# Kernel optimization log

Hardware: AMD Instinct MI355X
Metric: run time of the kernel (lower is better)

The kernel has to match this reference:

```python
import jax, jax.numpy as jnp
import numpy as np

B, N, K = 2, 2048, 30          # batch, residues, neighbors
DN, DE, L = 256, 128, 3        # dim_nodes, dim_edges, num_layers
NF, EF = 12, 28                # raw node / edge feature dims
EPS = 1e-6


def _gather(h, idx):
    # h: [B,N,D], idx: [B,N,K] -> [B,N,K,D]
    b, n, k = idx.shape
    d = h.shape[-1]
    return jnp.take_along_axis(h, idx.reshape(b, n * k, 1), axis=1).reshape(b, n, k, d)


def _nrm(v):
    return v / (jnp.linalg.norm(v, axis=-1, keepdims=True) + EPS)


def _forward(X, C, Wn, bn, We, be, Wm1, bm1, Wm2, bm2, Wue1, bue1, Wue2, bue2):
    mask_i = (C > 0).astype(X.dtype)                      # [B,N]
    Nat, CA, Cat, Oat = X[..., 0, :], X[..., 1, :], X[..., 2, :], X[..., 3, :]

    # local residue frames via Gram-Schmidt on (N, CA, C)
    u = _nrm(Cat - CA)
    v0 = Nat - CA
    v = _nrm(v0 - jnp.sum(v0 * u, -1, keepdims=True) * u)
    w = jnp.cross(u, v)
    R = jnp.stack([u, v, w], axis=-1)                     # [B,N,3,3]

    # node features: internal coords (unit bond vectors + log lengths)
    def bond_feat(bv):
        return jnp.concatenate([_nrm(bv), jnp.log(jnp.linalg.norm(bv, axis=-1, keepdims=True) + EPS)], -1)
    node_feat = jnp.concatenate([bond_feat(CA - Nat), bond_feat(Cat - CA), bond_feat(Oat - Cat)], -1)  # [B,N,12]
    node_h = (node_feat @ Wn + bn) * mask_i[..., None]

    # kNN graph on centroid distances (graph_distance_atom_type=-1)
    Xc = X.mean(axis=2)                                   # [B,N,3]
    D2 = jnp.sum((Xc[:, :, None] - Xc[:, None, :]) ** 2, -1)  # [B,N,N]
    BIG = 1e9
    D2 = D2 + BIG * (1.0 - mask_i)[:, None, :] + BIG * jnp.eye(N, dtype=X.dtype)[None]
    _, edge_idx = jax.lax.top_k(-D2, K)                   # [B,N,K]

    mask_j = _gather(mask_i[..., None], edge_idx)[..., 0]
    mask_ij = mask_i[..., None] * mask_j                  # [B,N,K]

    # edge features: RBF distances + local-frame direction + relative rotation
    xj = _gather(Xc, edge_idx)
    d = xj - Xc[:, :, None]                               # [B,N,K,3]
    dist = jnp.linalg.norm(d, axis=-1)
    local = jnp.einsum('bndc,bnkd->bnkc', R, d)           # R_i^T d
    dirv = local / (dist[..., None] + EPS)
    Rj = _gather(R.reshape(B, N, 9), edge_idx).reshape(B, N, K, 3, 3)
    Rrel = jnp.einsum('bnde,bnkdf->bnkef', R, Rj).reshape(B, N, K, 9)  # R_i^T R_j
    centers = jnp.linspace(0.0, 20.0, 16)
    sigma = 20.0 / 16.0
    rbf = jnp.exp(-(((dist[..., None] - centers) / sigma) ** 2))       # [B,N,K,16]
    edge_h = (jnp.concatenate([rbf, dirv, Rrel], -1) @ We + be) * mask_ij[..., None]

    # GNN message passing: gather -> MLP -> masked mean scatter, + edge update
    denom = jnp.sum(mask_ij, -1, keepdims=True) + EPS     # [B,N,1]
    for l in range(L):
        hj = _gather(node_h, edge_idx)                    # [B,N,K,DN]
        hi = jnp.broadcast_to(node_h[:, :, None], hj.shape)
        mi = jnp.concatenate([hi, hj, edge_h], -1)        # [B,N,K,2*DN+DE]
        m = jax.nn.softplus(mi @ Wm1[l] + bm1[l]) @ Wm2[l] + bm2[l]
        m = m * mask_ij[..., None]
        node_h = (node_h + m.sum(axis=2) / denom) * mask_i[..., None]
        e = jax.nn.softplus(mi @ Wue1[l] + bue1[l]) @ Wue2[l] + bue2[l]
        edge_h = (edge_h + e) * mask_ij[..., None]

    return node_h, edge_h, edge_idx, mask_i, mask_ij


def setup_inputs() -> dict:
    key = jax.random.key(0)
    ks = jax.random.split(key, 10)
    s = lambda i, shp: jax.random.normal(ks[i], shp, jnp.float32) * 0.05
    M = 2 * DN + DE
    inp = {
        'X': jax.random.normal(ks[0], (B, N, 4, 3), jnp.float32),
        'C': jax.random.randint(ks[1], (B, N), 0, 4),
        'Wn': s(2, (NF, DN)), 'bn': jnp.zeros((DN,), jnp.float32),
        'We': s(3, (EF, DE)), 'be': jnp.zeros((DE,), jnp.float32),
        'Wm1': s(4, (L, M, DN)), 'bm1': jnp.zeros((L, DN), jnp.float32),
        'Wm2': s(5, (L, DN, DN)), 'bm2': jnp.zeros((L, DN), jnp.float32),
        'Wue1': s(6, (L, M, DE)), 'bue1': jnp.zeros((L, DE), jnp.float32),
        'Wue2': s(7, (L, DE, DE)), 'bue2': jnp.zeros((L, DE), jnp.float32),
    }
    return inp


def reference(X, C, Wn, bn, We, be, Wm1, bm1, Wm2, bm2, Wue1, bue1, Wue2, bue2):
    return _forward(X, C, Wn, bn, We, be, Wm1, bm1, Wm2, bm2, Wue1, bue1, Wue2, bue2)
```

## Files before the change

### kernel.cpp

```cpp
#include <hip/hip_runtime.h>
#include <math.h>

#define Bdim 2
#define Nn   2048
#define Kn   30
#define KP   32
#define DNc  256
#define DEc  128
#define NODES (Bdim*Nn)
#define EDGES (Bdim*Nn*Kn)
#define RPAD  (NODES*KP)
#define EPSF 1e-6f

#define BK 64
#define LDA (BK+8)
#define LDA0 40
#define LDP 136

typedef __attribute__((ext_vector_type(8))) short short8;
typedef __attribute__((ext_vector_type(4))) short sh4;
typedef __attribute__((ext_vector_type(4))) float floatx4;

__device__ __forceinline__ float softplusf(float x){
    float e = __expf(-fabsf(x));
    return fmaxf(x, 0.f) + __logf(1.f + e);
}

__device__ __forceinline__ unsigned short f2bf(float x){
    union { float f; unsigned u; } v; v.f = x;
    unsigned r = v.u + 0x7fff + ((v.u >> 16) & 1);
    return (unsigned short)(r >> 16);
}
__device__ __forceinline__ float bf2f(unsigned short h){
    union { unsigned u; float f; } v; v.u = ((unsigned)h) << 16;
    return v.f;
}

__global__ __launch_bounds__(256) void k_geom(
    const float* __restrict__ X, const int* __restrict__ C,
    float* __restrict__ Xc, float* __restrict__ Rm,
    float* __restrict__ feat, float* __restrict__ mask_out)
{
    int id = blockIdx.x*256 + threadIdx.x;
    if (id >= NODES) return;
    float a[4][3];
    #pragma unroll
    for (int t=0;t<4;++t)
        #pragma unroll
        for (int d=0;d<3;++d) a[t][d] = X[id*12 + t*3 + d];
    #pragma unroll
    for (int d=0; d<3; ++d){
        float s = __fadd_rn(__fadd_rn(__fadd_rn(a[0][d],a[1][d]),a[2][d]),a[3][d]);
        Xc[id*3+d] = __fmul_rn(s, 0.25f);
    }
    mask_out[id] = (C[id] > 0) ? 1.f : 0.f;

    float u[3], v[3], w[3], b2[3], v0[3], vv[3];
    #pragma unroll
    for (int d=0;d<3;++d) b2[d] = a[2][d]-a[1][d];
    float n2 = sqrtf(b2[0]*b2[0]+b2[1]*b2[1]+b2[2]*b2[2]);
    #pragma unroll
    for (int d=0;d<3;++d) u[d] = b2[d]/(n2+EPSF);
    #pragma unroll
    for (int d=0;d<3;++d) v0[d] = a[0][d]-a[1][d];
    float dt = v0[0]*u[0]+v0[1]*u[1]+v0[2]*u[2];
    #pragma unroll
    for (int d=0;d<3;++d) vv[d] = v0[d] - dt*u[d];
    float nv = sqrtf(vv[0]*vv[0]+vv[1]*vv[1]+vv[2]*vv[2]);
    #pragma unroll
    for (int d=0;d<3;++d) v[d] = vv[d]/(nv+EPSF);
    w[0] = u[1]*v[2]-u[2]*v[1];
    w[1] = u[2]*v[0]-u[0]*v[2];
    w[2] = u[0]*v[1]-u[1]*v[0];
    #pragma unroll
    for (int d=0;d<3;++d){
        Rm[id*9 + d*3 + 0] = u[d];
        Rm[id*9 + d*3 + 1] = v[d];
        Rm[id*9 + d*3 + 2] = w[d];
    }
    float bonds[3][3];
    #pragma unroll
    for (int d=0;d<3;++d){
        bonds[0][d] = a[1][d]-a[0][d];
        bonds[1][d] = b2[d];
        bonds[2][d] = a[3][d]-a[2][d];
    }
    #pragma unroll
    for (int bi=0;bi<3;++bi){
        float nb = sqrtf(bonds[bi][0]*bonds[bi][0]+bonds[bi][1]*bonds[bi][1]+bonds[bi][2]*bonds[bi][2]);
        #pragma unroll
        for (int d=0;d<3;++d) feat[id*12 + bi*4 + d] = bonds[bi][d]/(nb+EPSF);
        feat[id*12 + bi*4 + 3] = logf(nb+EPSF);
    }
}

__global__ __launch_bounds__(256) void k_nodeh(
    const float* __restrict__ feat, const float* __restrict__ Wn,
    const float* __restrict__ bn, const int* __restrict__ C,
    float* __restrict__ node_h, unsigned short* __restrict__ node_bf)
{
    int nid = blockIdx.x;
    int c   = threadIdx.x;
    __shared__ float f[12];
    if (c < 12) f[c] = feat[nid*12 + c];
    __syncthreads();
    float acc = bn[c];
    #pragma unroll
    for (int k=0;k<12;++k) acc += f[k]*Wn[k*DNc + c];
    float mask = (C[nid] > 0) ? 1.f : 0.f;
    float r = acc*mask;
    node_h[nid*DNc + c] = r;
    node_bf[nid*DNc + c] = f2bf(r);
}

__global__ __launch_bounds__(256) void k_knn(
    const float* __restrict__ Xc, const int* __restrict__ C,
    int* __restrict__ eidx, float* __restrict__ eidx_f)
{
    __shared__ float sx[Nn], sy[Nn], sz[Nn], sadd[Nn];
    int tid  = threadIdx.x;
    int lane = tid & 63, wave = tid >> 6;
    int node0 = blockIdx.x*4;
    int base  = (node0 >> 11) << 11;
    for (int j=tid; j<Nn; j+=256){
        int gj = base + j;
        sx[j] = Xc[gj*3+0]; sy[j] = Xc[gj*3+1]; sz[j] = Xc[gj*3+2];
        sadd[j] = (C[gj] > 0) ? 0.f : 1e9f;
    }
    __syncthreads();

    int node = node0 + wave;
    int iloc = node & (Nn-1);
    float xi = sx[iloc], yi = sy[iloc], zi = sz[iloc];

    unsigned long long kreg[32];
    unsigned long long gm[8];
    #pragma unroll
    for (int t=0; t<32; ++t){
        int j = lane + t*64;
        float dx = __fsub_rn(xi, sx[j]);
        float dy = __fsub_rn(yi, sy[j]);
        float dz = __fsub_rn(zi, sz[j]);
        float vv = __fadd_rn(__fadd_rn(__fmul_rn(dx,dx),__fmul_rn(dy,dy)),__fmul_rn(dz,dz));
        vv = __fadd_rn(vv, sadd[j]);
        if (j == iloc) vv = __fadd_rn(vv, 1e9f);
        union { float f; unsigned u; } cv; cv.f = vv;
        kreg[t] = (((unsigned long long)cv.u) << 11) | (unsigned)j;
    }
    #pragma unroll
    for (int g=0; g<8; ++g){
        unsigned long long a = kreg[4*g+0], b = kreg[4*g+1];
        unsigned long long c = kreg[4*g+2], d = kreg[4*g+3];
        unsigned long long m1 = a<b?a:b, m2 = c<d?c:d;
        gm[g] = m1<m2?m1:m2;
    }
    unsigned long long m = gm[0]; int marg = 0;
    #pragma unroll
    for (int g=1; g<8; ++g) if (gm[g] < m){ m = gm[g]; marg = g; }

    for (int kk=0; kk<Kn; ++kk){
        unsigned long long best = m;
        #pragma unroll
        for (int d=1; d<64; d<<=1){
            unsigned long long o = __shfl_xor(best, d, 64);
            if (o < best) best = o;
        }
        if (lane == 0){
            int j = (int)(best & 2047ull);
            eidx  [(size_t)node*Kn + kk] = j;
            eidx_f[(size_t)node*Kn + kk] = (float)j;
        }
        if (m == best){
            #pragma unroll
            for (int g=0; g<8; ++g){
                if (marg == g){
                    #pragma unroll
                    for (int t=0; t<4; ++t)
                        if (kreg[4*g+t] == best) kreg[4*g+t] = ~0ull;
                    unsigned long long a = kreg[4*g+0], b = kreg[4*g+1];
                    unsigned long long c = kreg[4*g+2], d = kreg[4*g+3];
                    unsigned long long m1 = a<b?a:b, m2 = c<d?c:d;
                    gm[g] = m1<m2?m1:m2;
                }
            }
            m = gm[0]; marg = 0;
            #pragma unroll
            for (int g=1; g<8; ++g) if (gm[g] < m){ m = gm[g]; marg = g; }
        }
    }
}

__global__ __launch_bounds__(256) void k_edge_feat(
    const float* __restrict__ Xc, const float* __restrict__ Rm,
    const int* __restrict__ eidx, const int* __restrict__ C,
    unsigned short* __restrict__ featp,
    float* __restrict__ mask_ij_out, float* __restrict__ mask_pad,
    int* __restrict__ jg_pad, float* __restrict__ cnt)
{
    int r   = blockIdx.x*256 + threadIdx.x;
    int nid = r >> 5;
    int k   = r & 31;
    int b   = nid >> 11;
    float mij = 0.f;
    int   jb  = nid;
    float f[28];
    if (k < Kn){
        int e = nid*Kn + k;
        int j = eidx[e];
        jb = (b<<11) + j;
        mij = (C[nid] > 0 && C[jb] > 0) ? 1.f : 0.f;
        mask_ij_out[e] = mij;
        float xi0 = Xc[nid*3+0], xi1 = Xc[nid*3+1], xi2 = Xc[nid*3+2];
        float d0  = Xc[jb*3+0]-xi0;
        float d1  = Xc[jb*3+1]-xi1;
        float d2v = Xc[jb*3+2]-xi2;
        float dist = sqrtf(d0*d0 + d1*d1 + d2v*d2v);
        float ri[9], rj[9];
        #pragma unroll
        for (int q=0;q<9;++q) ri[q] = Rm[nid*9+q];
        #pragma unroll
        for (int q=0;q<9;++q) rj[q] = Rm[jb*9+q];
        #pragma unroll
        for (int c=0; c<16; ++c){
            float ctr = (20.f/15.f)*(float)c;
            float t = (dist - ctr)*(1.f/1.25f);
            f[c] = expf(-t*t);
        }
        #pragma unroll
        for (int cc=0; cc<3; ++cc){
            float loc = ri[0*3+cc]*d0 + ri[1*3+cc]*d1 + ri[2*3+cc]*d2v;
            f[16+cc] = loc/(dist+EPSF);
        }
        #pragma unroll
        for (int ee=0; ee<3; ++ee)
            #pragma unroll
            for (int ff=0; ff<3; ++ff)
                f[19+ee*3+ff] = ri[0+ee]*rj[0+ff] + ri[3+ee]*rj[3+ff] + ri[6+ee]*rj[6+ff];
    }
    jg_pad[r]   = jb;
    mask_pad[r] = mij;

    unsigned long long bal = __ballot(mij > 0.f);
    int lane = threadIdx.x & 63;
    if (lane == 0)  cnt[r >> 5] = (float)__popcll(bal & 0xFFFFFFFFull);
    if (lane == 32) cnt[r >> 5] = (float)__popcll(bal >> 32);

    unsigned short ov[32];
    #pragma unroll
    for (int q=0;q<32;++q) ov[q] = 0;
    if (k < Kn){
        #pragma unroll
        for (int q=0;q<28;++q) ov[q] = f2bf(f[q]);
    }
    unsigned short* dst = featp + (size_t)r*32;
    #pragma unroll
    for (int q=0; q<4; ++q){
        short8 sv;
        #pragma unroll
        for (int z=0; z<8; ++z) sv[z] = (short)ov[q*8+z];
        *(short8*)(dst + q*8) = sv;
    }
}

__global__ __launch_bounds__(256) void k_edge0(
    const unsigned short* __restrict__ featp, const unsigned short* __restrict__ Wp,
    const float* __restrict__ be, const float* __restrict__ mask_pad,
    unsigned short* __restrict__ edge_pad)
{
    __shared__ __align__(16) unsigned short smem[128*LDP];
    __shared__ float smask[128];
    unsigned short* Als  = smem;
    unsigned short* Bls  = smem + 128*LDA0;
    unsigned short* tile = smem;

    int tid = threadIdx.x;
    int lane = tid & 63, wave = tid >> 6;
    int wm = wave >> 1, wn = wave & 1;

    {
        const unsigned short* Ab = featp + (size_t)blockIdx.x*128*32;
        #pragma unroll
        for (int it=0; it<2; ++it){
            int idx = it*256 + tid;
            int row = idx >> 2, q = idx & 3;
            *(float4*)(&Als[row*LDA0 + q*8]) = *(const float4*)(Ab + row*32 + q*8);
        }
        if (tid < 128){
            int row = tid;
            *(float4*)(&Bls[row*LDA0 + 0])  = *(const float4*)(Wp + row*32 + 0);
            *(float4*)(&Bls[row*LDA0 + 8])  = *(const float4*)(Wp + row*32 + 8);
            *(float4*)(&Bls[row*LDA0 + 16]) = *(const float4*)(Wp + row*32 + 16);
            *(float4*)(&Bls[row*LDA0 + 24]) = *(const float4*)(Wp + row*32 + 24);
        } else {
            smask[tid-128] = mask_pad[blockIdx.x*128 + (tid-128)];
        }
    }
    __syncthreads();

    floatx4 acc[4][4];
    #pragma unroll
    for (int i=0;i<4;++i)
        #pragma unroll
        for (int j=0;j<4;++j) acc[i][j] = (floatx4){0.f,0.f,0.f,0.f};
    short8 af[4], bf[4];
    int kidx = (lane>>4)*8;
    #pragma unroll
    for (int t=0;t<4;++t){
        int row = wm*64 + t*16 + (lane&15);
        af[t] = *(const short8*)(&Als[row*LDA0 + kidx]);
        int col = wn*64 + t*16 + (lane&15);
        bf[t] = *(const short8*)(&Bls[col*LDA0 + kidx]);
    }
    __syncthreads();
    #pragma unroll
    for (int i=0;i<4;++i)
        #pragma unroll
        for (int j=0;j<4;++j)
            acc[i][j] = __builtin_amdgcn_mfma_f32_16x16x32_bf16(bf[j], af[i], acc[i][j], 0,0,0);

    int quad = lane >> 4, cl = lane & 15;
    #pragma unroll
    for (int i=0;i<4;++i){
        int rowl = wm*64 + i*16 + cl;
        float mk = smask[rowl];
        #pragma unroll
        for (int j=0;j<4;++j){
            int coll = wn*64 + j*16 + quad*4;
            float4 bv = *(const float4*)&be[coll];
            sh4 w;
            w[0] = (short)f2bf((acc[i][j][0] + bv.x)*mk);
            w[1] = (short)f2bf((acc[i][j][1] + bv.y)*mk);
            w[2] = (short)f2bf((acc[i][j][2] + bv.z)*mk);
            w[3] = (short)f2bf((acc[i][j][3] + bv.w)*mk);
            *(sh4*)(&tile[rowl*LDP + coll]) = w;
        }
    }
    __syncthreads();
    {
        int rl = tid >> 1;
        int h  = tid & 1;
        unsigned short* dst = edge_pad + (size_t)(blockIdx.x*128 + rl)*128 + h*64;
        #pragma unroll
        for (int q=0; q<8; ++q)
            *(short8*)(dst + q*8) = *(const short8*)(&tile[rl*LDP + h*64 + q*8]);
    }
}

__global__ __launch_bounds__(256) void k_pack_all(
    const float* __restrict__ We, const float* __restrict__ Wm1,
    const float* __restrict__ Wue1, const float* __restrict__ Wue2,
    const float* __restrict__ Wm2,
    unsigned short* __restrict__ wWe0, unsigned short* __restrict__ wPQw,
    unsigned short* __restrict__ wEw, unsigned short* __restrict__ wUe2w,
    unsigned short* __restrict__ wM2w)
{
    int id = blockIdx.x*256 + threadIdx.x;
    if (id < 4096){
        int n = id >> 5, kk = id & 31;
        wWe0[id] = (kk < 28) ? f2bf(We[kk*128 + n]) : 0;
        return;
    }
    id -= 4096;
    if (id < 3*768*256){
        int l = id / (768*256);
        int rem = id % (768*256);
        int n = rem >> 8, k = rem & 255;
        int c = (n < 384) ? n : n - 384;
        int r = (n < 384) ? k : 256 + k;
        float v = (c < 256) ? Wm1[((size_t)l*640 + r)*256 + c]
                            : Wue1[((size_t)l*640 + r)*128 + (c-256)];
        wPQw[id] = f2bf(v);
        return;
    }
    id -= 3*768*256;
    if (id < 3*384*128){
        int l = id / (384*128);
        int rem = id % (384*128);
        int n = rem >> 7, k = rem & 127;
        int r = 512 + k;
        float v = (n < 256) ? Wm1[((size_t)l*640 + r)*256 + n]
                            : Wue1[((size_t)l*640 + r)*128 + (n-256)];
        wEw[id] = f2bf(v);
        return;
    }
    id -= 3*384*128;
    if (id < 3*128*128){
        int l = id / (128*128);
        int rem = id % (128*128);
        int n = rem >> 7, k = rem & 127;
        wUe2w[id] = f2bf(Wue2[((size_t)l*128 + k)*128 + n]);
        return;
    }
    id -= 3*128*128;
    if (id < 3*256*256){
        int l = id / (256*256);
        int rem = id % (256*256);
        int n = rem >> 8, k = rem & 255;
        wM2w[id] = f2bf(Wm2[((size_t)l*256 + k)*256 + n]);
    }
}

template<int NR>
__device__ __forceinline__ void stage_tile_t(
    const unsigned short* __restrict__ gbase, int ldg, int k0,
    unsigned short* lds, int tid)
{
    #pragma unroll
    for (int it=0; it<NR/32; ++it){
        int idx = it*256 + tid;
        int row = idx >> 3;
        int ke  = (idx & 7) * 8;
        const float4* src = (const float4*)(gbase + (size_t)row*ldg + k0 + ke);
        *(float4*)(&lds[row*LDA + ke]) = *src;
    }
}

template<int TI, int TJ>
__device__ __forceinline__ void mma_tile_t(
    const unsigned short* Als, const unsigned short* Bls,
    int wm, int wn, int lane, floatx4 acc[TI][TJ])
{
    #pragma unroll
    for (int s=0; s<2; ++s){
        short8 af[TI], bf[TJ];
        int kidx = s*32 + (lane>>4)*8;
        #pragma unroll
        for (int t=0;t<TI;++t){
            int row = wm*(TI*16) + t*16 + (lane&15);
            af[t] = *(const short8*)(&Als[row*LDA + kidx]);
        }
        #pragma unroll
        for (int t=0;t<TJ;++t){
            int col = wn*(TJ*16) + t*16 + (lane&15);
            bf[t] = *(const short8*)(&Bls[col*LDA + kidx]);
        }
        #pragma unroll
        for (int i=0;i<TI;++i)
            #pragma unroll
            for (int j=0;j<TJ;++j)
                acc[i][j] = __builtin_amdgcn_mfma_f32_16x16x32_bf16(af[i], bf[j], acc[i][j], 0,0,0);
    }
}

template<int TI, int TJ>
__device__ __forceinline__ void mma_tile_sw(
    const unsigned short* Als, const unsigned short* Bls,
    int wm, int wn, int lane, floatx4 acc[TI][TJ])
{
    #pragma unroll
    for (int s=0; s<2; ++s){
        short8 af[TI], bf[TJ];
        int kidx = s*32 + (lane>>4)*8;
        #pragma unroll
        for (int t=0;t<TI;++t){
            int row = wm*(TI*16) + t*16 + (lane&15);
            af[t] = *(const short8*)(&Als[row*LDA + kidx]);
        }
        #pragma unroll
        for (int t=0;t<TJ;++t){
            int col = wn*(TJ*16) + t*16 + (lane&15);
            bf[t] = *(const short8*)(&Bls[col*LDA + kidx]);
        }
        #pragma unroll
        for (int i=0;i<TI;++i)
            #pragma unroll
            for (int j=0;j<TJ;++j)
                acc[i][j] = __builtin_amdgcn_mfma_f32_16x16x32_bf16(bf[j], af[i], acc[i][j], 0,0,0);
    }
}

__device__ __forceinline__ void mma_tileA_gB(
    const unsigned short* Atile, const unsigned short* __restrict__ Bg,
    int k0, int wm, int wn, int lane, floatx4 acc[4][4])
{
    #pragma unroll
    for (int s=0; s<2; ++s){
        short8 af[4], bf[4];
        int kloc = s*32 + (lane>>4)*8;
        #pragma unroll
        for (int t=0;t<4;++t){
            int row = wm*64 + t*16 + (lane&15);
            af[t] = *(const short8*)(&Atile[row*LDP + k0 + kloc]);
            int col = wn*64 + t*16 + (lane&15);
            bf[t] = *(const short8*)(Bg + (size_t)col*128 + k0 + kloc);
        }
        #pragma unroll
        for (int i=0;i<4;++i)
            #pragma unroll
            for (int j=0;j<4;++j)
                acc[i][j] = __builtin_amdgcn_mfma_f32_16x16x32_bf16(af[i], bf[j], acc[i][j], 0,0,0);
    }
}

__global__ __launch_bounds__(256) void k_pq(
    const unsigned short* __restrict__ A, const unsigned short* __restrict__ Bw,
    unsigned short* __restrict__ PQbf,
    const float* __restrict__ bm1l, const float* __restrict__ bue1l)
{
    __shared__ __align__(16) unsigned short smem[2*64*LDA];
    unsigned short* Als = smem;
    unsigned short* Bls = smem + 64*LDA;
    unsigned short* tile = smem;
    int tid = threadIdx.x;
    int lane = tid & 63, wave = tid >> 6;
    int wm = wave >> 1, wn = wave & 1;
    const unsigned short* Ab = A + (size_t)blockIdx.x*64*256;
    const unsigned short* Bb = Bw + (size_t)blockIdx.y*64*256;
    floatx4 acc[2][2];
    #pragma unroll
    for (int i=0;i<2;++i)
        #pragma unroll
        for (int j=0;j<2;++j) acc[i][j] = (floatx4){0.f,0.f,0.f,0.f};
    for (int k0=0; k0<256; k0+=BK){
        stage_tile_t<64>(Ab, 256, k0, Als, tid);
        stage_tile_t<64>(Bb, 256, k0, Bls, tid);
        __syncthreads();
        mma_tile_sw<2,2>(Als, Bls, wm, wn, lane, acc);
        __syncthreads();
    }
    int quad = lane >> 4, cl = lane & 15;
    #pragma unroll
    for (int i=0;i<2;++i){
        int rowl = wm*32 + i*16 + cl;
        #pragma unroll
        for (int j=0;j<2;++j){
            int coll = wn*32 + j*16 + quad*4;
            int col0 = blockIdx.y*64 + coll;
            float4 bv;
            if (col0 < 256)      bv = *(const float4*)&bm1l[col0];
            else if (col0 < 384) bv = *(const float4*)&bue1l[col0-256];
            else                 bv = (float4){0.f,0.f,0.f,0.f};
            sh4 w;
            w[0] = (short)f2bf(acc[i][j][0] + bv.x);
            w[1] = (short)f2bf(acc[i][j][1] + bv.y);
            w[2] = (short)f2bf(acc[i][j][2] + bv.z);
            w[3] = (short)f2bf(acc[i][j][3] + bv.w);
            *(sh4*)(&tile[rowl*LDP + coll]) = w;
        }
    }
    __syncthreads();
    {
        int rl = tid >> 2;
        int h  = tid & 3;
        unsigned short* dst = PQbf + (size_t)(blockIdx.x*64 + rl)*768 + blockIdx.y*64 + h*16;
        *(short8*)(dst + 0) = *(const short8*)(&tile[rl*LDP + h*16 + 0]);
        *(short8*)(dst + 8) = *(const short8*)(&tile[rl*LDP + h*16 + 8]);
    }
}

__global__ __launch_bounds__(256) void k_h1s(
    const unsigned short* __restrict__ Apad, const unsigned short* __restrict__ Bw,
    const unsigned short* __restrict__ PQbf, const int* __restrict__ jg_pad,
    const float* __restrict__ mask_pad,
    unsigned short* __restrict__ Sout)
{
    __shared__ __align__(16) unsigned short smem[2*128*LDA];
    __shared__ float smask[128];
    unsigned short* Als = smem;
    unsigned short* Bls = smem + 128*LDA;
    unsigned short* pqT = smem;

    int tid = threadIdx.x;
    int lane = tid & 63, wave = tid >> 6;
    int wm = wave >> 1, wn = wave & 1;
    int colblk = blockIdx.y;

    const unsigned short* Ab = Apad + (size_t)blockIdx.x*128*128;
    const unsigned short* Bb = Bw + (size_t)colblk*128*128;
    floatx4 acc[4][4];
    #pragma unroll
    for (int i=0;i<4;++i)
        #pragma unroll
        for (int j=0;j<4;++j) acc[i][j] = (floatx4){0.f,0.f,0.f,0.f};
    for (int k0=0; k0<128; k0+=BK){
        stage_tile_t<128>(Ab, 128, k0, Als, tid);
        stage_tile_t<128>(Bb, 128, k0, Bls, tid);
        __syncthreads();
        mma_tile_t<4,4>(Als, Bls, wm, wn, lane, acc);
        __syncthreads();
    }

    {
        int colbase = colblk*128;
        #pragma unroll
        for (int it=0; it<2; ++it){
            int w    = it*256 + tid;
            int rq   = w & 31;
            int c8   = w >> 5;
            int row0 = rq*4;
            int r0   = blockIdx.x*128 + row0;
            int ni   = r0 >> 5;
            int4 jg4 = *(const int4*)&jg_pad[r0];
            int colg = colbase + c8*8;
            short8 pv = *(const short8*)(PQbf + (size_t)ni*768 + colg);
            short8 q0 = *(const short8*)(PQbf + (size_t)jg4.x*768 + 384 + colg);
            short8 q1 = *(const short8*)(PQbf + (size_t)jg4.y*768 + 384 + colg);
            short8 q2 = *(const short8*)(PQbf + (size_t)jg4.z*768 + 384 + colg);
            short8 q3 = *(const short8*)(PQbf + (size_t)jg4.w*768 + 384 + colg);
            #pragma unroll
            for (int q=0; q<8; ++q){
                float pf = bf2f((unsigned short)pv[q]);
                sh4 ov;
                ov[0] = (short)f2bf(pf + bf2f((unsigned short)q0[q]));
                ov[1] = (short)f2bf(pf + bf2f((unsigned short)q1[q]));
                ov[2] = (short)f2bf(pf + bf2f((unsigned short)q2[q]));
                ov[3] = (short)f2bf(pf + bf2f((unsigned short)q3[q]));
                *(sh4*)(&pqT[(c8*8 + q)*LDP + row0]) = ov;
            }
        }
        if (tid < 128) smask[tid] = mask_pad[blockIdx.x*128 + tid];
    }
    __syncthreads();

    int quad = lane >> 4, cl = lane & 15;
    float sumA[4] = {0.f,0.f,0.f,0.f};
    float sumB[4] = {0.f,0.f,0.f,0.f};
    #pragma unroll
    for (int i=0;i<4;++i){
        int rowl0 = wm*64 + i*16 + quad*4;
        float4 mk = *(const float4*)&smask[rowl0];
        float mkv[4] = {mk.x, mk.y, mk.z, mk.w};
        #pragma unroll
        for (int j=0;j<4;++j){
            int coll = wn*64 + j*16 + cl;
            sh4 pq4 = *(const sh4*)(&pqT[coll*LDP + rowl0]);
            #pragma unroll
            for (int rg=0; rg<4; ++rg){
                float v  = softplusf(acc[i][j][rg] + bf2f((unsigned short)pq4[rg]));
                float mv = mkv[rg]*v;
                if (i < 2) sumA[j] += mv; else sumB[j] += mv;
            }
        }
    }

    int nodeA = blockIdx.x*4 + wm*2;
    #pragma unroll
    for (int j=0;j<4;++j){
        float a = sumA[j];
        a += __shfl_xor(a, 16, 64);
        a += __shfl_xor(a, 32, 64);
        float b = sumB[j];
        b += __shfl_xor(b, 16, 64);
        b += __shfl_xor(b, 32, 64);
        int col = colblk*128 + wn*64 + j*16 + cl;
        if (quad == 0)      Sout[(size_t)nodeA*256 + col]     = f2bf(a);
        else if (quad == 1) Sout[(size_t)(nodeA+1)*256 + col] = f2bf(b);
    }
}

__global__ __launch_bounds__(256) void k_h1e(
    const unsigned short* __restrict__ Apad, const unsigned short* __restrict__ BwE,
    const unsigned short* __restrict__ BwU2,
    const unsigned short* __restrict__ PQbf, const int* __restrict__ jg_pad,
    const float* __restrict__ mask_pad, const float* __restrict__ bue2l,
    unsigned short* __restrict__ edge_pad, float* __restrict__ edge_f32,
    int last)
{
    __shared__ __align__(16) unsigned short smem[2*128*LDA];
    __shared__ float sbias[128];
    unsigned short* Als  = smem;
    unsigned short* Bls  = smem + 128*LDA;
    unsigned short* tile = smem;

    int tid = threadIdx.x;
    int lane = tid & 63, wave = tid >> 6;
    int wm = wave >> 1, wn = wave & 1;

    if (tid < 128) sbias[tid] = bue2l[tid];

    const unsigned short* Ab = Apad + (size_t)blockIdx.x*128*128;
    floatx4 acc[4][4];
    #pragma unroll
    for (int i=0;i<4;++i)
        #pragma unroll
        for (int j=0;j<4;++j) acc[i][j] = (floatx4){0.f,0.f,0.f,0.f};
    for (int k0=0; k0<128; k0+=BK){
        stage_tile_t<128>(Ab, 128, k0, Als, tid);
        stage_tile_t<128>(BwE, 128, k0, Bls, tid);
        __syncthreads();
        mma_tile_t<4,4>(Als, Bls, wm, wn, lane, acc);
        __syncthreads();
    }

    {
        int rl = tid >> 1;
        int h  = tid & 1;
        int r  = blockIdx.x*128 + rl;
        int ni = r >> 5;
        int jg = jg_pad[r];
        int cb = 256 + h*64;
        const unsigned short* Pr = PQbf + (size_t)ni*768 + cb;
        const unsigned short* Qr = PQbf + (size_t)jg*768 + 384 + cb;
        #pragma unroll
        for (int q=0; q<8; ++q){
            short8 pv = *(const short8*)(Pr + q*8);
            short8 qv = *(const short8*)(Qr + q*8);
            short8 ov;
            #pragma unroll
            for (int z=0; z<8; ++z)
                ov[z] = (short)f2bf(bf2f((unsigned short)pv[z]) + bf2f((unsigned short)qv[z]));
            *(short8*)(&tile[rl*LDP + h*64 + q*8]) = ov;
        }
    }
    __syncthreads();

    int quad = lane >> 4, cl = lane & 15;
    #pragma unroll
    for (int i=0;i<4;++i){
        #pragma unroll
        for (int rg=0;rg<4;++rg){
            int rowl = wm*64 + i*16 + quad*4 + rg;
            #pragma unroll
            for (int j=0;j<4;++j){
                int coll = wn*64 + j*16 + cl;
                float pq = bf2f(tile[rowl*LDP + coll]);
                float v  = softplusf(acc[i][j][rg] + pq);
                tile[rowl*LDP + coll] = f2bf(v);
            }
        }
    }
    __syncthreads();

    floatx4 acc2[4][4];
    #pragma unroll
    for (int i=0;i<4;++i)
        #pragma unroll
        for (int j=0;j<4;++j) acc2[i][j] = (floatx4){0.f,0.f,0.f,0.f};
    mma_tileA_gB(tile, BwU2, 0,  wm, wn, lane, acc2);
    mma_tileA_gB(tile, BwU2, 64, wm, wn, lane, acc2);
    __syncthreads();

    #pragma unroll
    for (int i=0;i<4;++i){
        #pragma unroll
        for (int rg=0;rg<4;++rg){
            int rowl = wm*64 + i*16 + quad*4 + rg;
            #pragma unroll
            for (int j=0;j<4;++j){
                int coll = wn*64 + j*16 + cl;
                tile[rowl*LDP + coll] = f2bf(acc2[i][j][rg]);
            }
        }
    }
    __syncthreads();

    if (last){
        int c16  = lane & 31;
        int rsub = lane >> 5;
        #pragma unroll
        for (int step=0; step<16; ++step){
            int rowl = wave*32 + step*2 + rsub;
            int R = blockIdx.x*128 + rowl;
            int k = R & (KP-1);
            if (k < Kn){
                float mij = mask_pad[R];
                int node = R >> 5;
                int e = node*Kn + k;
                sh4 ov = *(const sh4*)(edge_pad + (size_t)R*128 + c16*4);
                sh4 av = *(const sh4*)(&tile[rowl*LDP + c16*4]);
                float4 bv = *(const float4*)(&sbias[c16*4]);
                float4 f;
                f.x = (bf2f((unsigned short)ov[0]) + bf2f((unsigned short)av[0]) + bv.x)*mij;
                f.y = (bf2f((unsigned short)ov[1]) + bf2f((unsigned short)av[1]) + bv.y)*mij;
                f.z = (bf2f((unsigned short)ov[2]) + bf2f((unsigned short)av[2]) + bv.z)*mij;
                f.w = (bf2f((unsigned short)ov[3]) + bf2f((unsigned short)av[3]) + bv.w)*mij;
                *(float4*)(edge_f32 + (size_t)e*128 + c16*4) = f;
            }
        }
    } else {
        int c8   = lane & 15;
        int rsub = lane >> 4;
        #pragma unroll
        for (int step=0; step<8; ++step){
            int rowl = wave*32 + step*4 + rsub;
            int R = blockIdx.x*128 + rowl;
            int k = R & (KP-1);
            if (k < Kn){
                float mij = mask_pad[R];
                unsigned short* ep = edge_pad + (size_t)R*128 + c8*8;
                short8 ov = *(const short8*)ep;
                short8 av = *(const short8*)(&tile[rowl*LDP + c8*8]);
                float4 b0 = *(const float4*)(&sbias[c8*8]);
                float4 b1 = *(const float4*)(&sbias[c8*8 + 4]);
                float nv[8];
                nv[0] = (bf2f((unsigned short)ov[0]) + bf2f((unsigned short)av[0]) + b0.x)*mij;
                nv[1] = (bf2f((unsigned short)ov[1]) + bf2f((unsigned short)av[1]) + b0.y)*mij;
                nv[2] = (bf2f((unsigned short)ov[2]) + bf2f((unsigned short)av[2]) + b0.z)*mij;
                nv[3] = (bf2f((unsigned short)ov[3]) + bf2f((unsigned short)av[3]) + b0.w)*mij;
                nv[4] = (bf2f((unsigned short)ov[4]) + bf2f((unsigned short)av[4]) + b1.x)*mij;
                nv[5] = (bf2f((unsigned short)ov[5]) + bf2f((unsigned short)av[5]) + b1.y)*mij;
                nv[6] = (bf2f((unsigned short)ov[6]) + bf2f((unsigned short)av[6]) + b1.z)*mij;
                nv[7] = (bf2f((unsigned short)ov[7]) + bf2f((unsigned short)av[7]) + b1.w)*mij;
                short8 sv;
                #pragma unroll
                for (int z=0; z<8; ++z) sv[z] = (short)f2bf(nv[z]);
                *(short8*)ep = sv;
            }
        }
    }
}

__global__ __launch_bounds__(256) void k_node_gemm(
    const unsigned short* __restrict__ S, const unsigned short* __restrict__ Bw,
    const float* __restrict__ bm2l, const float* __restrict__ cnt,
    const float* __restrict__ mask_i,
    float* __restrict__ node_h, unsigned short* __restrict__ node_bf)
{
    __shared__ __align__(16) unsigned short Als[32*LDA];
    __shared__ __align__(16) unsigned short Bls[64*LDA];
    int tid = threadIdx.x;
    int lane = tid & 63, wave = tid >> 6;
    int wm = wave >> 1, wn = wave & 1;
    const unsigned short* Ab = S + (size_t)blockIdx.x*32*256;
    const unsigned short* Bb = Bw + (size_t)blockIdx.y*64*256;
    floatx4 acc[1][2];
    acc[0][0] = (floatx4){0.f,0.f,0.f,0.f};
    acc[0][1] = (floatx4){0.f,0.f,0.f,0.f};
    for (int k0=0; k0<256; k0+=BK){
        stage_tile_t<32>(Ab, 256, k0, Als, tid);
        stage_tile_t<64>(Bb, 256, k0, Bls, tid);
        __syncthreads();
        mma_tile_sw<1,2>(Als, Bls, wm, wn, lane, acc);
        __syncthreads();
    }
    int quad = lane >> 4, cl = lane & 15;
    {
        int nid = blockIdx.x*32 + wm*16 + cl;
        float ct = cnt[nid];
        float mi = mask_i[nid];
        float dv = ct + EPSF;
        #pragma unroll
        for (int j=0;j<2;++j){
            int col = blockIdx.y*64 + wn*32 + j*16 + quad*4;
            float4 bv = *(const float4*)&bm2l[col];
            float4 nh = *(const float4*)&node_h[(size_t)nid*256 + col];
            float4 r;
            r.x = (nh.x + (acc[0][j][0] + ct*bv.x)/dv)*mi;
            r.y = (nh.y + (acc[0][j][1] + ct*bv.y)/dv)*mi;
            r.z = (nh.z + (acc[0][j][2] + ct*bv.z)/dv)*mi;
            r.w = (nh.w + (acc[0][j][3] + ct*bv.w)/dv)*mi;
            *(float4*)&node_h[(size_t)nid*256 + col] = r;
            sh4 w;
            w[0] = (short)f2bf(r.x);
            w[1] = (short)f2bf(r.y);
            w[2] = (short)f2bf(r.z);
            w[3] = (short)f2bf(r.w);
            *(sh4*)&node_bf[(size_t)nid*256 + col] = w;
        }
    }
}

extern "C" void kernel_launch(void* const* d_in, const int* in_sizes, int n_in,
                              void* d_out, int out_size, void* d_ws, size_t ws_size,
                              hipStream_t stream)
{
    (void)in_sizes; (void)n_in; (void)out_size; (void)ws_size;
    const float* X   = (const float*)d_in[0];
    const int*   C   = (const int*)  d_in[1];
    const float* Wn  = (const float*)d_in[2];
    const float* bn  = (const float*)d_in[3];
    const float* We  = (const float*)d_in[4];
    const float* be  = (const float*)d_in[5];
    const float* Wm1 = (const float*)d_in[6];
    const float* bm1 = (const float*)d_in[7];
    const float* Wm2 = (const float*)d_in[8];
    const float* bm2 = (const float*)d_in[9];
    const float* Wue1= (const float*)d_in[10];
    const float* bue1= (const float*)d_in[11];
    const float* Wue2= (const float*)d_in[12];
    const float* bue2= (const float*)d_in[13];

    float* out       = (float*)d_out;
    float* out_node  = out;
    float* out_edge  = out + 1048576;
    float* out_eidxf = out + 16777216;
    float* out_maski = out + 16900096;
    float* out_maskij= out + 16904192;

    char* wsb = (char*)d_ws;
    size_t off = 0;
    float* wXc    = (float*)(wsb + off); off += (size_t)12288*4;
    float* wR     = (float*)(wsb + off); off += (size_t)36864*4;
    float* wF     = (float*)(wsb + off); off += (size_t)49152*4;
    int*   wEidx  = (int*)  (wsb + off); off += (size_t)EDGES*4;
    int*   wJgPad = (int*)  (wsb + off); off += (size_t)RPAD*4;
    float* wMaskP = (float*)(wsb + off); off += (size_t)RPAD*4;
    float* wCnt   = (float*)(wsb + off); off += (size_t)NODES*4;
    unsigned short* wPQ      = (unsigned short*)(wsb + off); off += (size_t)NODES*768*2;
    unsigned short* wS       = (unsigned short*)(wsb + off); off += (size_t)NODES*256*2;
    unsigned short* wNodeBf  = (unsigned short*)(wsb + off); off += (size_t)NODES*256*2;
    unsigned short* wEdgePad = (unsigned short*)(wsb + off); off += (size_t)RPAD*128*2;
    unsigned short* wFeatP   = (unsigned short*)(wsb + off); off += (size_t)RPAD*32*2;
    unsigned short* wWe0     = (unsigned short*)(wsb + off); off += (size_t)128*32*2;
    unsigned short* wPQw     = (unsigned short*)(wsb + off); off += (size_t)3*768*256*2;
    unsigned short* wEw      = (unsigned short*)(wsb + off); off += (size_t)3*384*128*2;
    unsigned short* wUe2w    = (unsigned short*)(wsb + off); off += (size_t)3*128*128*2;
    unsigned short* wM2w     = (unsigned short*)(wsb + off); off += (size_t)3*256*256*2;

    k_geom <<<16,    256, 0, stream>>>(X, C, wXc, wR, wF, out_maski);
    k_nodeh<<<NODES, 256, 0, stream>>>(wF, Wn, bn, C, out_node, wNodeBf);
    k_knn  <<<NODES/4, 256, 0, stream>>>(wXc, C, wEidx, out_eidxf);

    k_pack_all<<<3856, 256, 0, stream>>>(We, Wm1, Wue1, Wue2, Wm2,
                                         wWe0, wPQw, wEw, wUe2w, wM2w);
    k_edge_feat<<<RPAD/256, 256, 0, stream>>>(wXc, wR, wEidx, C, wFeatP,
                                              out_maskij, wMaskP, wJgPad, wCnt);
    k_edge0<<<RPAD/128, 256, 0, stream>>>(wFeatP, wWe0, be, wMaskP, wEdgePad);

    for (int l=0; l<3; ++l){
        k_pq<<<dim3(64,12), 256, 0, stream>>>(wNodeBf, wPQw + (size_t)l*768*256, wPQ,
                                              bm1 + l*256, bue1 + l*128);
        k_h1s<<<dim3(RPAD/128,2), 256, 0, stream>>>(
            wEdgePad, wEw + (size_t)l*384*128, wPQ, wJgPad, wMaskP, wS);
        k_h1e<<<RPAD/128, 256, 0, stream>>>(
            wEdgePad, wEw + (size_t)l*384*128 + (size_t)256*128,
            wUe2w + (size_t)l*128*128, wPQ, wJgPad, wMaskP, bue2 + l*128,
            wEdgePad, out_edge, (l==2) ? 1 : 0);
        k_node_gemm<<<dim3(NODES/32,4), 256, 0, stream>>>(
            wS, wM2w + (size_t)l*256*256, bm2 + l*256, wCnt, out_maski,
            out_node, wNodeBf);
    }
}
```

Before: 448.0 us.

## Merge node-sum and edge-update kernels into one launch with ping-pong edge buffers

The separate k_h1s (node message sum, two column blocks) and k_h1e (edge update) launches are combined into a single kernel whose blocks pick a role from the block index. The block ordering is arranged so the three roles for the same edge tile share an XCD, letting the A tile be reused from that XCD's L2. Because edge-update blocks now run alongside blocks that still read the edge tensor, the edge state is double-buffered, and padding rows are written as zeros. This saves one launch per layer and lets the two kinds of work overlap, at the cost of an extra edge buffer and divergent block roles.

```diff
diff --git a/kernel.cpp b/kernel.cpp
--- a/kernel.cpp
+++ b/kernel.cpp
@@ -548,253 +548,254 @@
     }
 }
 
-__global__ __launch_bounds__(256) void k_h1s(
-    const unsigned short* __restrict__ Apad, const unsigned short* __restrict__ Bw,
+__global__ __launch_bounds__(256) void k_h1f(
+    const unsigned short* __restrict__ Apad,
+    const unsigned short* __restrict__ BwAll,
+    const unsigned short* __restrict__ BwU2,
     const unsigned short* __restrict__ PQbf, const int* __restrict__ jg_pad,
-    const float* __restrict__ mask_pad,
-    unsigned short* __restrict__ Sout)
+    const float* __restrict__ mask_pad, const float* __restrict__ bue2l,
+    unsigned short* __restrict__ Sout,
+    unsigned short* __restrict__ edge_nxt, float* __restrict__ edge_f32,
+    int last)
 {
     __shared__ __align__(16) unsigned short smem[2*128*LDA];
-    __shared__ float smask[128];
-    unsigned short* Als = smem;
-    unsigned short* Bls = smem + 128*LDA;
-    unsigned short* pqT = smem;
+    __shared__ float saux[128];
+
+    int g    = blockIdx.x;
+    int xcd  = g & 7;
+    int grp  = g >> 3;
+    int role = grp % 3;
+    int bx   = (grp/3)*8 + xcd;
 
     int tid = threadIdx.x;
     int lane = tid & 63, wave = tid >> 6;
     int wm = wave >> 1, wn = wave & 1;
-    int colblk = blockIdx.y;
-
-    const unsigned short* Ab = Apad + (size_t)blockIdx.x*128*128;
-    const unsigned short* Bb = Bw + (size_t)colblk*128*128;
-    floatx4 acc[4][4];
-    #pragma unroll
-    for (int i=0;i<4;++i)
-        #pragma unroll
-        for (int j=0;j<4;++j) acc[i][j] = (floatx4){0.f,0.f,0.f,0.f};
-    for (int k0=0; k0<128; k0+=BK){
-        stage_tile_t<128>(Ab, 128, k0, Als, tid);
-        stage_tile_t<128>(Bb, 128, k0, Bls, tid);
+    int quad = lane >> 4, cl = lane & 15;
+
+    if (role < 2){
+        unsigned short* Als = smem;
+        unsigned short* Bls = smem + 128*LDA;
+        unsigned short* pqT = smem;
+        int colblk = role;
+
+        const unsigned short* Ab = Apad + (size_t)bx*128*128;
+        const unsigned short* Bb = BwAll + (size_t)colblk*128*128;
+        floatx4 acc[4][4];
+        #pragma unroll
+        for (int i=0;i<4;++i)
+            #pragma unroll
+            for (int j=0;j<4;++j) acc[i][j] = (floatx4){0.f,0.f,0.f,0.f};
+        for (int k0=0; k0<128; k0+=BK){
+            stage_tile_t<128>(Ab, 128, k0, Als, tid);
+            stage_tile_t<128>(Bb, 128, k0, Bls, tid);
+            __syncthreads();
+            mma_tile_t<4,4>(Als, Bls, wm, wn, lane, acc);
+            __syncthreads();
+        }
+
+        {
+            int colbase = colblk*128;
+            #pragma unroll
+            for (int it=0; it<2; ++it){
+                int w    = it*256 + tid;
+                int rq   = w & 31;
+                int c8   = w >> 5;
+                int row0 = rq*4;
+                int r0   = bx*128 + row0;
+                int ni   = r0 >> 5;
+                int4 jg4 = *(const int4*)&jg_pad[r0];
+                int colg = colbase + c8*8;
+                short8 pv = *(const short8*)(PQbf + (size_t)ni*768 + colg);
+                short8 q0 = *(const short8*)(PQbf + (size_t)jg4.x*768 + 384 + colg);
+                short8 q1 = *(const short8*)(PQbf + (size_t)jg4.y*768 + 384 + colg);
+                short8 q2 = *(const short8*)(PQbf + (size_t)jg4.z*768 + 384 + colg);
+                short8 q3 = *(const short8*)(PQbf + (size_t)jg4.w*768 + 384 + colg);
+                #pragma unroll
+                for (int q=0; q<8; ++q){
+                    float pf = bf2f((unsigned short)pv[q]);
+                    sh4 ov;
+                    ov[0] = (short)f2bf(pf + bf2f((unsigned short)q0[q]));
+                    ov[1] = (short)f2bf(pf + bf2f((unsigned short)q1[q]));
+                    ov[2] = (short)f2bf(pf + bf2f((unsigned short)q2[q]));
+                    ov[3] = (short)f2bf(pf + bf2f((unsigned short)q3[q]));
+                    *(sh4*)(&pqT[(c8*8 + q)*LDP + row0]) = ov;
+                }
+            }
+            if (tid < 128) saux[tid] = mask_pad[bx*128 + tid];
+        }
         __syncthreads();
-        mma_tile_t<4,4>(Als, Bls, wm, wn, lane, acc);
-        __syncthreads();
-    }
-
-    {
-        int colbase = colblk*128;
-        #pragma unroll
-        for (int it=0; it<2; ++it){
-            int w    = it*256 + tid;
-            int rq   = w & 31;
-            int c8   = w >> 5;
-            int row0 = rq*4;
-            int r0   = blockIdx.x*128 + row0;
-            int ni   = r0 >> 5;
-            int4 jg4 = *(const int4*)&jg_pad[r0];
-            int colg = colbase + c8*8;
-            short8 pv = *(const short8*)(PQbf + (size_t)ni*768 + colg);
-            short8 q0 = *(const short8*)(PQbf + (size_t)jg4.x*768 + 384 + colg);
-            short8 q1 = *(const short8*)(PQbf + (size_t)jg4.y*768 + 384 + colg);
-            short8 q2 = *(const short8*)(PQbf + (size_t)jg4.z*768 + 384 + colg);
-            short8 q3 = *(const short8*)(PQbf + (size_t)jg4.w*768 + 384 + colg);
-            #pragma unroll
-            for (int q=0; q<8; ++q){
-                float pf = bf2f((unsigned short)pv[q]);
-                sh4 ov;
-                ov[0] = (short)f2bf(pf + bf2f((unsigned short)q0[q]));
-                ov[1] = (short)f2bf(pf + bf2f((unsigned short)q1[q]));
-                ov[2] = (short)f2bf(pf + bf2f((unsigned short)q2[q]));
-                ov[3] = (short)f2bf(pf + bf2f((unsigned short)q3[q]));
-                *(sh4*)(&pqT[(c8*8 + q)*LDP + row0]) = ov;
-            }
-        }
-        if (tid < 128) smask[tid] = mask_pad[blockIdx.x*128 + tid];
-    }
-    __syncthreads();
-
-    int quad = lane >> 4, cl = lane & 15;
-    float sumA[4] = {0.f,0.f,0.f,0.f};
-    float sumB[4] = {0.f,0.f,0.f,0.f};
-    #pragma unroll
-    for (int i=0;i<4;++i){
-        int rowl0 = wm*64 + i*16 + quad*4;
-        float4 mk = *(const float4*)&smask[rowl0];
-        float mkv[4] = {mk.x, mk.y, mk.z, mk.w};
-        #pragma unroll
-        for (int j=0;j<4;++j){
-            int coll = wn*64 + j*16 + cl;
-            sh4 pq4 = *(const sh4*)(&pqT[coll*LDP + rowl0]);
-            #pragma unroll
-            for (int rg=0; rg<4; ++rg){
-                float v  = softplusf(acc[i][j][rg] + bf2f((unsigned short)pq4[rg]));
-                float mv = mkv[rg]*v;
-                if (i < 2) sumA[j] += mv; else sumB[j] += mv;
-            }
-        }
-    }
-
-    int nodeA = blockIdx.x*4 + wm*2;
-    #pragma unroll
-    for (int j=0;j<4;++j){
-        float a = sumA[j];
-        a += __shfl_xor(a, 16, 64);
-        a += __shfl_xor(a, 32, 64);
-        float b = sumB[j];
-        b += __shfl_xor(b, 16, 64);
-        b += __shfl_xor(b, 32, 64);
-        int col = colblk*128 + wn*64 + j*16 + cl;
-        if (quad == 0)      Sout[(size_t)nodeA*256 + col]     = f2bf(a);
-        else if (quad == 1) Sout[(size_t)(nodeA+1)*256 + col] = f2bf(b);
-    }
-}
-
-__global__ __launch_bounds__(256) void k_h1e(
-    const unsigned short* __restrict__ Apad, const unsigned short* __restrict__ BwE,
-    const unsigned short* __restrict__ BwU2,
-    const unsigned short* __restrict__ PQbf, const int* __restrict__ jg_pad,
-    const float* __restrict__ mask_pad, const float* __restrict__ bue2l,
-    unsigned short* __restrict__ edge_pad, float* __restrict__ edge_f32,
-    int last)
-{
-    __shared__ __align__(16) unsigned short smem[2*128*LDA];
-    __shared__ float sbias[128];
-    unsigned short* Als  = smem;
-    unsigned short* Bls  = smem + 128*LDA;
-    unsigned short* tile = smem;
-
-    int tid = threadIdx.x;
-    int lane = tid & 63, wave = tid >> 6;
-    int wm = wave >> 1, wn = wave & 1;
-
-    if (tid < 128) sbias[tid] = bue2l[tid];
-
-    const unsigned short* Ab = Apad + (size_t)blockIdx.x*128*128;
-    floatx4 acc[4][4];
-    #pragma unroll
-    for (int i=0;i<4;++i)
-        #pragma unroll
-        for (int j=0;j<4;++j) acc[i][j] = (floatx4){0.f,0.f,0.f,0.f};
-    for (int k0=0; k0<128; k0+=BK){
-        stage_tile_t<128>(Ab, 128, k0, Als, tid);
-        stage_tile_t<128>(BwE, 128, k0, Bls, tid);
-        __syncthreads();
-        mma_tile_t<4,4>(Als, Bls, wm, wn, lane, acc);
-        __syncthreads();
-    }
-
-    {
-        int rl = tid >> 1;
-        int h  = tid & 1;
-        int r  = blockIdx.x*128 + rl;
-        int ni = r >> 5;
-        int jg = jg_pad[r];
-        int cb = 256 + h*64;
-        const unsigned short* Pr = PQbf + (size_t)ni*768 + cb;
-        const unsigned short* Qr = PQbf + (size_t)jg*768 + 384 + cb;
-        #pragma unroll
-        for (int q=0; q<8; ++q){
-            short8 pv = *(const short8*)(Pr + q*8);
-            short8 qv = *(const short8*)(Qr + q*8);
-            short8 ov;
-            #pragma unroll
-            for (int z=0; z<8; ++z)
-                ov[z] = (short)f2bf(bf2f((unsigned short)pv[z]) + bf2f((unsigned short)qv[z]));
-            *(short8*)(&tile[rl*LDP + h*64 + q*8]) = ov;
-        }
-    }
-    __syncthreads();
-
-    int quad = lane >> 4, cl = lane & 15;
-    #pragma unroll
-    for (int i=0;i<4;++i){
-        #pragma unroll
-        for (int rg=0;rg<4;++rg){
-            int rowl = wm*64 + i*16 + quad*4 + rg;
+
+        float sumA[4] = {0.f,0.f,0.f,0.f};
+        float sumB[4] = {0.f,0.f,0.f,0.f};
+        #pragma unroll
+        for (int i=0;i<4;++i){
+            int rowl0 = wm*64 + i*16 + quad*4;
+            float4 mk = *(const float4*)&saux[rowl0];
+            float mkv[4] = {mk.x, mk.y, mk.z, mk.w};
             #pragma unroll
             for (int j=0;j<4;++j){
                 int coll = wn*64 + j*16 + cl;
-                float pq = bf2f(tile[rowl*LDP + coll]);
-                float v  = softplusf(acc[i][j][rg] + pq);
-                tile[rowl*LDP + coll] = f2bf(v);
+                sh4 pq4 = *(const sh4*)(&pqT[coll*LDP + rowl0]);
+                #pragma unroll
+                for (int rg=0; rg<4; ++rg){
+                    float v  = softplusf(acc[i][j][rg] + bf2f((unsigned short)pq4[rg]));
+                    float mv = mkv[rg]*v;
+                    if (i < 2) sumA[j] += mv; else sumB[j] += mv;
+                }
             }
         }
-    }
-    __syncthreads();
-
-    floatx4 acc2[4][4];
-    #pragma unroll
-    for (int i=0;i<4;++i)
-        #pragma unroll
-        for (int j=0;j<4;++j) acc2[i][j] = (floatx4){0.f,0.f,0.f,0.f};
-    mma_tileA_gB(tile, BwU2, 0,  wm, wn, lane, acc2);
-    mma_tileA_gB(tile, BwU2, 64, wm, wn, lane, acc2);
-    __syncthreads();
-
-    #pragma unroll
-    for (int i=0;i<4;++i){
-        #pragma unroll
-        for (int rg=0;rg<4;++rg){
-            int rowl = wm*64 + i*16 + quad*4 + rg;
-            #pragma unroll
-            for (int j=0;j<4;++j){
-                int coll = wn*64 + j*16 + cl;
-                tile[rowl*LDP + coll] = f2bf(acc2[i][j][rg]);
+
+        int nodeA = bx*4 + wm*2;
+        #pragma unroll
+        for (int j=0;j<4;++j){
+            float a = sumA[j];
+            a += __shfl_xor(a, 16, 64);
+            a += __shfl_xor(a, 32, 64);
+            float b = sumB[j];
+            b += __shfl_xor(b, 16, 64);
+            b += __shfl_xor(b, 32, 64);
+            int col = colblk*128 + wn*64 + j*16 + cl;
+            if (quad == 0)      Sout[(size_t)nodeA*256 + col]     = f2bf(a);
+            else if (quad == 1) Sout[(size_t)(nodeA+1)*256 + col] = f2bf(b);
+        }
+    } else {
+        unsigned short* Als  = smem;
+        unsigned short* Bls  = smem + 128*LDA;
+        unsigned short* tile = smem;
+        const unsigned short* BwE = BwAll + (size_t)2*128*128;
+
+        if (tid < 128) saux[tid] = bue2l[tid];
+
+        const unsigned short* Ab = Apad + (size_t)bx*128*128;
+        floatx4 acc[4][4];
+        #pragma unroll
+        for (int i=0;i<4;++i)
+            #pragma unroll
+            for (int j=0;j<4;++j) acc[i][j] = (floatx4){0.f,0.f,0.f,0.f};
+        for (int k0=0; k0<128; k0+=BK){
+            stage_tile_t<128>(Ab, 128, k0, Als, tid);
+            stage_tile_t<128>(BwE, 128, k0, Bls, tid);
+            __syncthreads();
+            mma_tile_t<4,4>(Als, Bls, wm, wn, lane, acc);
+            __syncthreads();
+        }
+
+        {
+            int rl = tid >> 1;
+            int h  = tid & 1;
+            int r  = bx*128 + rl;
+            int ni = r >> 5;
+            int jg = jg_pad[r];
+            int cb = 256 + h*64;
+            const unsigned short* Pr = PQbf + (size_t)ni*768 + cb;
+            const unsigned short* Qr = PQbf + (size_t)jg*768 + 384 + cb;
+            #pragma unroll
+            for (int q=0; q<8; ++q){
+                short8 pv = *(const short8*)(Pr + q*8);
+                short8 qv = *(const short8*)(Qr + q*8);
+                short8 ov;
+                #pragma unroll
+                for (int z=0; z<8; ++z)
+                    ov[z] = (short)f2bf(bf2f((unsigned short)pv[z]) + bf2f((unsigned short)qv[z]));
+                *(short8*)(&tile[rl*LDP + h*64 + q*8]) = ov;
             }
         }
-    }
-    __syncthreads();
-
-    if (last){
-        int c16  = lane & 31;
-        int rsub = lane >> 5;
-        #pragma unroll
-        for (int step=0; step<16; ++step){
-            int rowl = wave*32 + step*2 + rsub;
-            int R = blockIdx.x*128 + rowl;
-            int k = R & (KP-1);
-            if (k < Kn){
-                float mij = mask_pad[R];
-                int node = R >> 5;
-                int e = node*Kn + k;
-                sh4 ov = *(const sh4*)(edge_pad + (size_t)R*128 + c16*4);
-                sh4 av = *(const sh4*)(&tile[rowl*LDP + c16*4]);
-                float4 bv = *(const float4*)(&sbias[c16*4]);
-                float4 f;
-                f.x = (bf2f((unsigned short)ov[0]) + bf2f((unsigned short)av[0]) + bv.x)*mij;
-                f.y = (bf2f((unsigned short)ov[1]) + bf2f((unsigned short)av[1]) + bv.y)*mij;
-                f.z = (bf2f((unsigned short)ov[2]) + bf2f((unsigned short)av[2]) + bv.z)*mij;
-                f.w = (bf2f((unsigned short)ov[3]) + bf2f((unsigned short)av[3]) + bv.w)*mij;
-                *(float4*)(edge_f32 + (size_t)e*128 + c16*4) = f;
+        __syncthreads();
+
+        #pragma unroll
+        for (int i=0;i<4;++i){
+            #pragma unroll
+            for (int rg=0;rg<4;++rg){
+                int rowl = wm*64 + i*16 + quad*4 + rg;
+                #pragma unroll
+                for (int j=0;j<4;++j){
+                    int coll = wn*64 + j*16 + cl;
+                    float pq = bf2f(tile[rowl*LDP + coll]);
+                    float v  = softplusf(acc[i][j][rg] + pq);
+                    tile[rowl*LDP + coll] = f2bf(v);
+                }
             }
         }
-    } else {
-        int c8   = lane & 15;
-        int rsub = lane >> 4;
-        #pragma unroll
-        for (int step=0; step<8; ++step){
-            int rowl = wave*32 + step*4 + rsub;
-            int R = blockIdx.x*128 + rowl;
-            int k = R & (KP-1);
-            if (k < Kn){
-                float mij = mask_pad[R];
-                unsigned short* ep = edge_pad + (size_t)R*128 + c8*8;
-                short8 ov = *(const short8*)ep;
-                short8 av = *(const short8*)(&tile[rowl*LDP + c8*8]);
-                float4 b0 = *(const float4*)(&sbias[c8*8]);
-                float4 b1 = *(const float4*)(&sbias[c8*8 + 4]);
-                float nv[8];
-                nv[0] = (bf2f((unsigned short)ov[0]) + bf2f((unsigned short)av[0]) + b0.x)*mij;
-                nv[1] = (bf2f((unsigned short)ov[1]) + bf2f((unsigned short)av[1]) + b0.y)*mij;
-                nv[2] = (bf2f((unsigned short)ov[2]) + bf2f((unsigned short)av[2]) + b0.z)*mij;
-                nv[3] = (bf2f((unsigned short)ov[3]) + bf2f((unsigned short)av[3]) + b0.w)*mij;
-                nv[4] = (bf2f((unsigned short)ov[4]) + bf2f((unsigned short)av[4]) + b1.x)*mij;
-                nv[5] = (bf2f((unsigned short)ov[5]) + bf2f((unsigned short)av[5]) + b1.y)*mij;
-                nv[6] = (bf2f((unsigned short)ov[6]) + bf2f((unsigned short)av[6]) + b1.z)*mij;
-                nv[7] = (bf2f((unsigned short)ov[7]) + bf2f((unsigned short)av[7]) + b1.w)*mij;
-                short8 sv;
+        __syncthreads();
+
+        floatx4 acc2[4][4];
+        #pragma unroll
+        for (int i=0;i<4;++i)
+            #pragma unroll
+            for (int j=0;j<4;++j) acc2[i][j] = (floatx4){0.f,0.f,0.f,0.f};
+        mma_tileA_gB(tile, BwU2, 0,  wm, wn, lane, acc2);
+        mma_tileA_gB(tile, BwU2, 64, wm, wn, lane, acc2);
+        __syncthreads();
+
+        #pragma unroll
+        for (int i=0;i<4;++i){
+            #pragma unroll
+            for (int rg=0;rg<4;++rg){
+                int rowl = wm*64 + i*16 + quad*4 + rg;
                 #pragma unroll
-                for (int z=0; z<8; ++z) sv[z] = (short)f2bf(nv[z]);
-                *(short8*)ep = sv;
+                for (int j=0;j<4;++j){
+                    int coll = wn*64 + j*16 + cl;
+                    tile[rowl*LDP + coll] = f2bf(acc2[i][j][rg]);
+                }
+            }
+        }
+        __syncthreads();
+
+        if (last){
+            int c16  = lane & 31;
+            int rsub = lane >> 5;
+            #pragma unroll
+            for (int step=0; step<16; ++step){
+                int rowl = wave*32 + step*2 + rsub;
+                int R = bx*128 + rowl;
+                int k = R & (KP-1);
+                if (k < Kn){
+                    float mij = mask_pad[R];
+                    int node = R >> 5;
+                    int e = node*Kn + k;
+                    sh4 ov = *(const sh4*)(Apad + (size_t)R*128 + c16*4);
+                    sh4 av = *(const sh4*)(&tile[rowl*LDP + c16*4]);
+                    float4 bv = *(const float4*)(&saux[c16*4]);
+                    float4 f;
+                    f.x = (bf2f((unsigned short)ov[0]) + bf2f((unsigned short)av[0]) + bv.x)*mij;
+                    f.y = (bf2f((unsigned short)ov[1]) + bf2f((unsigned short)av[1]) + bv.y)*mij;
+                    f.z = (bf2f((unsigned short)ov[2]) + bf2f((unsigned short)av[2]) + bv.z)*mij;
+                    f.w = (bf2f((unsigned short)ov[3]) + bf2f((unsigned short)av[3]) + bv.w)*mij;
+                    *(float4*)(edge_f32 + (size_t)e*128 + c16*4) = f;
+                }
+            }
+        } else {
+            int c8   = lane & 15;
+            int rsub = lane >> 4;
+            #pragma unroll
+            for (int step=0; step<8; ++step){
+                int rowl = wave*32 + step*4 + rsub;
+                int R = bx*128 + rowl;
+                int k = R & (KP-1);
+                unsigned short* ep = edge_nxt + (size_t)R*128 + c8*8;
+                if (k < Kn){
+                    float mij = mask_pad[R];
+                    short8 ov = *(const short8*)(Apad + (size_t)R*128 + c8*8);
+                    short8 av = *(const short8*)(&tile[rowl*LDP + c8*8]);
+                    float4 b0 = *(const float4*)(&saux[c8*8]);
+                    float4 b1 = *(const float4*)(&saux[c8*8 + 4]);
+                    float nv[8];
+                    nv[0] = (bf2f((unsigned short)ov[0]) + bf2f((unsigned short)av[0]) + b0.x)*mij;
+                    nv[1] = (bf2f((unsigned short)ov[1]) + bf2f((unsigned short)av[1]) + b0.y)*mij;
+                    nv[2] = (bf2f((unsigned short)ov[2]) + bf2f((unsigned short)av[2]) + b0.z)*mij;
+                    nv[3] = (bf2f((unsigned short)ov[3]) + bf2f((unsigned short)av[3]) + b0.w)*mij;
+                    nv[4] = (bf2f((unsigned short)ov[4]) + bf2f((unsigned short)av[4]) + b1.x)*mij;
+                    nv[5] = (bf2f((unsigned short)ov[5]) + bf2f((unsigned short)av[5]) + b1.y)*mij;
+                    nv[6] = (bf2f((unsigned short)ov[6]) + bf2f((unsigned short)av[6]) + b1.z)*mij;
+                    nv[7] = (bf2f((unsigned short)ov[7]) + bf2f((unsigned short)av[7]) + b1.w)*mij;
+                    short8 sv;
+                    #pragma unroll
+                    for (int z=0; z<8; ++z) sv[z] = (short)f2bf(nv[z]);
+                    *(short8*)ep = sv;
+                } else {
+                    short8 z = {0,0,0,0,0,0,0,0};
+                    *(short8*)ep = z;
+                }
             }
         }
     }
@@ -889,7 +890,8 @@
     unsigned short* wPQ      = (unsigned short*)(wsb + off); off += (size_t)NODES*768*2;
     unsigned short* wS       = (unsigned short*)(wsb + off); off += (size_t)NODES*256*2;
     unsigned short* wNodeBf  = (unsigned short*)(wsb + off); off += (size_t)NODES*256*2;
-    unsigned short* wEdgePad = (unsigned short*)(wsb + off); off += (size_t)RPAD*128*2;
+    unsigned short* wEdgePadA= (unsigned short*)(wsb + off); off += (size_t)RPAD*128*2;
+    unsigned short* wEdgePadB= (unsigned short*)(wsb + off); off += (size_t)RPAD*128*2;
     unsigned short* wFeatP   = (unsigned short*)(wsb + off); off += (size_t)RPAD*32*2;
     unsigned short* wWe0     = (unsigned short*)(wsb + off); off += (size_t)128*32*2;
     unsigned short* wPQw     = (unsigned short*)(wsb + off); off += (size_t)3*768*256*2;
@@ -897,6 +899,8 @@
     unsigned short* wUe2w    = (unsigned short*)(wsb + off); off += (size_t)3*128*128*2;
     unsigned short* wM2w     = (unsigned short*)(wsb + off); off += (size_t)3*256*256*2;
 
+    unsigned short* eb[2] = { wEdgePadA, wEdgePadB };
+
     k_geom <<<16,    256, 0, stream>>>(X, C, wXc, wR, wF, out_maski);
     k_nodeh<<<NODES, 256, 0, stream>>>(wF, Wn, bn, C, out_node, wNodeBf);
     k_knn  <<<NODES/4, 256, 0, stream>>>(wXc, C, wEidx, out_eidxf);
@@ -905,17 +909,15 @@
                                          wWe0, wPQw, wEw, wUe2w, wM2w);
     k_edge_feat<<<RPAD/256, 256, 0, stream>>>(wXc, wR, wEidx, C, wFeatP,
                                               out_maskij, wMaskP, wJgPad, wCnt);
-    k_edge0<<<RPAD/128, 256, 0, stream>>>(wFeatP, wWe0, be, wMaskP, wEdgePad);
+    k_edge0<<<RPAD/128, 256, 0, stream>>>(wFeatP, wWe0, be, wMaskP, wEdgePadA);
 
     for (int l=0; l<3; ++l){
         k_pq<<<dim3(64,12), 256, 0, stream>>>(wNodeBf, wPQw + (size_t)l*768*256, wPQ,
                                               bm1 + l*256, bue1 + l*128);
-        k_h1s<<<dim3(RPAD/128,2), 256, 0, stream>>>(
-            wEdgePad, wEw + (size_t)l*384*128, wPQ, wJgPad, wMaskP, wS);
-        k_h1e<<<RPAD/128, 256, 0, stream>>>(
-            wEdgePad, wEw + (size_t)l*384*128 + (size_t)256*128,
-            wUe2w + (size_t)l*128*128, wPQ, wJgPad, wMaskP, bue2 + l*128,
-            wEdgePad, out_edge, (l==2) ? 1 : 0);
+        k_h1f<<<3*(RPAD/128), 256, 0, stream>>>(
+            eb[l&1], wEw + (size_t)l*384*128, wUe2w + (size_t)l*128*128,
+            wPQ, wJgPad, wMaskP, bue2 + l*128,
+            wS, eb[(l+1)&1], out_edge, (l==2) ? 1 : 0);
         k_node_gemm<<<dim3(NODES/32,4), 256, 0, stream>>>(
             wS, wM2w + (size_t)l*256*256, bm2 + l*256, wCnt, out_maski,
             out_node, wNodeBf);
```

Result: slower. 459.0 us (+2.4%).
